# Optimization experiments

Measured on AMD Instinct MI355X. Metric: run time of the kernel, lower is better.

The kernel has to match this reference:

```python
import jax, jax.numpy as jnp
import numpy as np

N_NODES = 100000
N_EDGES = 1600000
IN_FEATS, HIDDEN, N_CLASSES = 128, 64, 16


def gcn_layer(x, src, dst, W, b, n_nodes):
    # DGL GraphConv, norm='both': h = D_in^{-1/2} A (D_out^{-1/2} x) W + b
    # (W applied before aggregation since in_feats > out_feats, as DGL does)
    ones = jnp.ones((src.shape[0],), dtype=x.dtype)
    deg_out = jax.ops.segment_sum(ones, src, num_segments=n_nodes)
    deg_in = jax.ops.segment_sum(ones, dst, num_segments=n_nodes)
    norm_src = jax.lax.rsqrt(jnp.clip(deg_out, 1.0))  # [N]
    norm_dst = jax.lax.rsqrt(jnp.clip(deg_in, 1.0))   # [N]
    h = (x * norm_src[:, None]) @ W                    # [N, out]
    msgs = h[src]                                      # [E, out] gather
    agg = jax.ops.segment_sum(msgs, dst, num_segments=n_nodes)  # [N, out]
    return agg * norm_dst[:, None] + b


def setup_inputs() -> dict:
    key = jax.random.key(0)
    k1, k2, k3, k4, k5, k6, k7 = jax.random.split(key, 7)
    x = jax.random.normal(k1, (N_NODES, IN_FEATS), dtype=jnp.float32)
    src = jax.random.randint(k2, (N_EDGES,), 0, N_NODES, dtype=jnp.int32)
    dst = jax.random.randint(k3, (N_EDGES,), 0, N_NODES, dtype=jnp.int32)
    s1 = 1.0 / np.sqrt(IN_FEATS)
    s2 = 1.0 / np.sqrt(HIDDEN)
    W1 = jax.random.uniform(k4, (IN_FEATS, HIDDEN), jnp.float32, -s1, s1)
    b1 = jnp.zeros((HIDDEN,), dtype=jnp.float32)
    W2 = jax.random.uniform(k5, (HIDDEN, N_CLASSES), jnp.float32, -s2, s2)
    b2 = jnp.zeros((N_CLASSES,), dtype=jnp.float32)
    return {"x": x, "src": src, "dst": dst, "W1": W1, "b1": b1, "W2": W2, "b2": b2}


def reference(x, src, dst, W1, b1, W2, b2):
    h = gcn_layer(x, src, dst, W1, b1, N_NODES)
    h = jax.nn.relu(h)
    h = gcn_layer(h, src, dst, W2, b2, N_NODES)
    return jax.nn.softmax(h, axis=-1)  # [N, num_classes]
```

## Files before the change

kernel.cpp:

```cpp
#include <hip/hip_runtime.h>
#include <hip/hip_fp16.h>
#include <math.h>


constexpr int N_NODES = 100000;
constexpr int N_EDGES = 1600000;
constexpr int IN_F    = 128;
constexpr int HID     = 64;
constexpr int NC      = 16;

constexpr int NB_D   = 391;
constexpr int STR    = 4608;
constexpr int NBLK_P = 256;
constexpr int EPB    = N_EDGES / NBLK_P;
constexpr int CAPB   = 64;
constexpr int CSTR   = 16;

typedef _Float16 f16x8 __attribute__((ext_vector_type(8)));
typedef _Float16 f16x4 __attribute__((ext_vector_type(4)));
typedef float    f32x4 __attribute__((ext_vector_type(4)));

__global__ __launch_bounds__(512) void k_init(int* __restrict__ cursD,
                                              int* __restrict__ cursS) {
    int t = threadIdx.x;
    if (t < NB_D) {
        cursD[t * CSTR] = t * STR;
        cursS[t * CSTR] = t * STR;
    }
}

__global__ __launch_bounds__(1024) void k_part(const int* __restrict__ src,
                                               const int* __restrict__ dst,
                                               int* __restrict__ cursD,
                                               int* __restrict__ cursS,
                                               unsigned int* __restrict__ ebufD,
                                               unsigned char* __restrict__ ebufS) {
    __shared__ unsigned int  bufD[NB_D * CAPB];
    __shared__ unsigned char bufS[NB_D * CAPB];
    __shared__ int cD[NB_D], cS[NB_D], baseD[NB_D], baseS[NB_D];
    const int t = threadIdx.x, b = blockIdx.x;
    for (int i = t; i < NB_D; i += 1024) { cD[i] = 0; cS[i] = 0; }
    __syncthreads();
    const int beg = b * EPB, end = beg + EPB;
    for (int i = beg + t; i < end; i += 1024) {
        int d = dst[i], s = src[i];
        int bD = d >> 8;
        int c  = atomicAdd(&cD[bD], 1);
        if (c < CAPB) bufD[(bD << 6) + c] = ((unsigned)(d & 255) << 17) | (unsigned)s;
        int bS = s >> 8;
        int c2 = atomicAdd(&cS[bS], 1);
        if (c2 < CAPB) bufS[(bS << 6) + c2] = (unsigned char)(s & 255);
    }
    __syncthreads();
    for (int i = t; i < NB_D; i += 1024) {
        int c = min(cD[i], CAPB);
        cD[i] = c;
        baseD[i] = atomicAdd(&cursD[i * CSTR], c);
        int c2 = min(cS[i], CAPB);
        cS[i] = c2;
        baseS[i] = atomicAdd(&cursS[i * CSTR], c2);
    }
    __syncthreads();
    for (int slot = t; slot < NB_D * CAPB; slot += 1024) {
        int bk = slot >> 6, idx = slot & 63;
        if (idx < cD[bk]) ebufD[baseD[bk] + idx] = bufD[slot];
    }
    for (int slot = t; slot < NB_D * CAPB; slot += 1024) {
        int bk = slot >> 6, idx = slot & 63;
        if (idx < cS[bk]) ebufS[baseS[bk] + idx] = bufS[slot];
    }
}

__global__ __launch_bounds__(256) void k_bcsr(const int* __restrict__ cursD,
                                              const unsigned int* __restrict__ ebufD,
                                              int* __restrict__ row_start,
                                              int* __restrict__ row_end,
                                              float* __restrict__ norm_dst,
                                              int* __restrict__ csr_src) {
    __shared__ int cnt[256];
    __shared__ int curs[256];
    __shared__ int wsum[4];
    const int t = threadIdx.x, b = blockIdx.x;
    const int beg = b * STR, end = cursD[b * CSTR];
    cnt[t] = 0;
    __syncthreads();
    for (int i = beg + t; i < end; i += 256)
        atomicAdd(&cnt[ebufD[i] >> 17], 1);
    __syncthreads();
    int x = cnt[t];
    int v = x;
    int lane = t & 63, wid = t >> 6;
    #pragma unroll
    for (int d = 1; d < 64; d <<= 1) { int u = __shfl_up(v, d, 64); if (lane >= d) v += u; }
    if (lane == 63) wsum[wid] = v;
    __syncthreads();
    int woff = 0;
    for (int w = 0; w < wid; ++w) woff += wsum[w];
    int rs = woff + v - x;
    int node = b * 256 + t;
    if (node < N_NODES) {
        row_start[node] = beg + rs;
        row_end[node]   = beg + rs + x;
        norm_dst[node]  = 1.0f / sqrtf(fmaxf((float)x, 1.0f));
    }
    curs[t] = beg + rs;
    __syncthreads();
    for (int i = beg + t; i < end; i += 256) {
        unsigned int e = ebufD[i];
        int pos = atomicAdd(&curs[e >> 17], 1);
        csr_src[pos] = (int)(e & 0x1FFFFu);
    }
}

__global__ __launch_bounds__(256) void k_bdeg(const int* __restrict__ cursS,
                                              const unsigned char* __restrict__ ebufS,
                                              float* __restrict__ norm_src) {
    __shared__ int cnt[256];
    const int t = threadIdx.x, b = blockIdx.x;
    const int beg = b * STR, end = cursS[b * CSTR];
    cnt[t] = 0;
    __syncthreads();
    for (int i = beg + t; i < end; i += 256)
        atomicAdd(&cnt[ebufS[i]], 1);
    __syncthreads();
    int node = b * 256 + t;
    if (node < N_NODES)
        norm_src[node] = 1.0f / sqrtf(fmaxf((float)cnt[t], 1.0f));
}

constexpr int PADK = 136;
__global__ __launch_bounds__(256) void k_gemm1(
        const float* __restrict__ x, const float* __restrict__ W1,
        const float* __restrict__ norm_src, __half* __restrict__ h1h) {
    __shared__ _Float16 xh[64 * PADK];
    __shared__ _Float16 wt[64 * PADK];
    const int t = threadIdx.x;
    const int row0 = blockIdx.x * 64;
    for (int i = t; i < 64 * 32; i += 256) {
        int c4 = i & 31, rr = i >> 5;
        int gr = row0 + rr;
        float4 v = (gr < N_NODES) ? *(const float4*)&x[(size_t)gr * IN_F + c4 * 4]
                                  : float4{0.f, 0.f, 0.f, 0.f};
        f16x4 hv;
        hv[0] = (_Float16)v.x; hv[1] = (_Float16)v.y;
        hv[2] = (_Float16)v.z; hv[3] = (_Float16)v.w;
        *(f16x4*)&xh[rr * PADK + c4 * 4] = hv;
    }
    for (int i = t; i < 64 * 32; i += 256) {
        int n = i & 63, kq = i >> 6;
        int k0 = kq * 4;
        f16x4 hv;
        #pragma unroll
        for (int j = 0; j < 4; ++j)
            hv[j] = (_Float16)W1[(size_t)(k0 + j) * HID + n];
        *(f16x4*)&wt[n * PADK + k0] = hv;
    }
    __syncthreads();
    const int w = t >> 6;
    const int l = t & 63;
    const int m = l & 15, q = l >> 4;
    f32x4 acc0 = {0,0,0,0}, acc1 = {0,0,0,0}, acc2 = {0,0,0,0}, acc3 = {0,0,0,0};
    #pragma unroll
    for (int kc = 0; kc < 4; ++kc) {
        f16x8 af = *(const f16x8*)&xh[(16 * w + m) * PADK + kc * 32 + q * 8];
        f16x8 b0 = *(const f16x8*)&wt[( 0 + m) * PADK + kc * 32 + q * 8];
        f16x8 b1 = *(const f16x8*)&wt[(16 + m) * PADK + kc * 32 + q * 8];
        f16x8 b2 = *(const f16x8*)&wt[(32 + m) * PADK + kc * 32 + q * 8];
        f16x8 b3 = *(const f16x8*)&wt[(48 + m) * PADK + kc * 32 + q * 8];
        acc0 = __builtin_amdgcn_mfma_f32_16x16x32_f16(af, b0, acc0, 0, 0, 0);
        acc1 = __builtin_amdgcn_mfma_f32_16x16x32_f16(af, b1, acc1, 0, 0, 0);
        acc2 = __builtin_amdgcn_mfma_f32_16x16x32_f16(af, b2, acc2, 0, 0, 0);
        acc3 = __builtin_amdgcn_mfma_f32_16x16x32_f16(af, b3, acc3, 0, 0, 0);
    }
    _Float16* out = (_Float16*)h1h;
    #pragma unroll
    for (int r = 0; r < 4; ++r) {
        int row_g = row0 + 16 * w + q * 4 + r;
        if (row_g < N_NODES) {
            float ns = norm_src[row_g];
            size_t base = (size_t)row_g * HID + m;
            out[base +  0] = (_Float16)(acc0[r] * ns);
            out[base + 16] = (_Float16)(acc1[r] * ns);
            out[base + 32] = (_Float16)(acc2[r] * ns);
            out[base + 48] = (_Float16)(acc3[r] * ns);
        }
    }
}

__global__ __launch_bounds__(256) void k_agg1(
        const int* __restrict__ row_start, const int* __restrict__ row_end,
        const int* __restrict__ csr_src, const __half* __restrict__ h1h,
        const float* __restrict__ nd, const float* __restrict__ b1,
        float* __restrict__ h1r) {
    int node = blockIdx.x * 16 + (threadIdx.x >> 4);
    int q = threadIdx.x & 15;
    if (node >= N_NODES) return;
    int beg = row_start[node], end = row_end[node];
    float4 acc = {0.f, 0.f, 0.f, 0.f};
    int p = beg;
    for (; p + 8 <= end; p += 8) {
        float2 g[8];
        #pragma unroll
        for (int u = 0; u < 8; ++u) {
            int s = csr_src[p + u];
            g[u] = *(const float2*)&h1h[(size_t)s * HID + q * 4];
        }
        #pragma unroll
        for (int u = 0; u < 8; ++u) {
            float2 f0 = __half22float2(*(__half2*)&g[u].x);
            float2 f1 = __half22float2(*(__half2*)&g[u].y);
            acc.x += f0.x; acc.y += f0.y; acc.z += f1.x; acc.w += f1.y;
        }
    }
    for (; p < end; ++p) {
        int s = csr_src[p];
        float2 raw = *(const float2*)&h1h[(size_t)s * HID + q * 4];
        float2 f0 = __half22float2(*(__half2*)&raw.x);
        float2 f1 = __half22float2(*(__half2*)&raw.y);
        acc.x += f0.x; acc.y += f0.y; acc.z += f1.x; acc.w += f1.y;
    }
    float n = nd[node];
    float4 bb = *(const float4*)&b1[q * 4];
    float4 o;
    o.x = fmaxf(acc.x * n + bb.x, 0.f);
    o.y = fmaxf(acc.y * n + bb.y, 0.f);
    o.z = fmaxf(acc.z * n + bb.z, 0.f);
    o.w = fmaxf(acc.w * n + bb.w, 0.f);
    *(float4*)&h1r[(size_t)node * HID + q * 4] = o;
}

#define GEMM_STEP(accr, xvr) \
    accr.x += xvr.x*w0.x + xvr.y*w1.x + xvr.z*w2.x + xvr.w*w3.x; \
    accr.y += xvr.x*w0.y + xvr.y*w1.y + xvr.z*w2.y + xvr.w*w3.y; \
    accr.z += xvr.x*w0.z + xvr.y*w1.z + xvr.z*w2.z + xvr.w*w3.z; \
    accr.w += xvr.x*w0.w + xvr.y*w1.w + xvr.z*w2.w + xvr.w*w3.w;

__global__ __launch_bounds__(256) void k_gemm2(
        const float* __restrict__ hin, const float* __restrict__ W2,
        const float* __restrict__ norm_src, __half* __restrict__ h2h) {
    __shared__ float Ws[HID * NC];
    __shared__ float xs[64 * 68];
    const int t = threadIdx.x;
    for (int i = t * 4; i < HID * NC; i += 256 * 4)
        *(float4*)&Ws[i] = *(const float4*)&W2[i];
    const int jq = t & 3;
    const int rl = t >> 2;
    const int row0 = blockIdx.x * 64;
    __syncthreads();
    for (int i = t; i < 64 * (HID / 4); i += 256) {
        int rr = i >> 4, cc = i & 15;
        int gr = row0 + rr;
        float4 v = (gr < N_NODES) ? *(const float4*)&hin[(size_t)gr * HID + cc * 4]
                                  : float4{0.f, 0.f, 0.f, 0.f};
        *(float4*)&xs[rr * 68 + cc * 4] = v;
    }
    __syncthreads();
    int r = row0 + rl;
    if (r < N_NODES) {
        float4 acc = {0.f, 0.f, 0.f, 0.f};
        #pragma unroll
        for (int k = 0; k < HID; k += 4) {
            float4 xv = *(float4*)&xs[rl * 68 + k];
            float4 w0 = *(float4*)&Ws[(k + 0) * NC + jq * 4];
            float4 w1 = *(float4*)&Ws[(k + 1) * NC + jq * 4];
            float4 w2 = *(float4*)&Ws[(k + 2) * NC + jq * 4];
            float4 w3 = *(float4*)&Ws[(k + 3) * NC + jq * 4];
            GEMM_STEP(acc, xv)
        }
        float ns = norm_src[r];
        f16x4 hv;
        hv[0] = (_Float16)(acc.x * ns); hv[1] = (_Float16)(acc.y * ns);
        hv[2] = (_Float16)(acc.z * ns); hv[3] = (_Float16)(acc.w * ns);
        *(f16x4*)&((_Float16*)h2h)[(size_t)r * NC + jq * 4] = hv;
    }
}

__global__ __launch_bounds__(256) void k_agg2(
        const int* __restrict__ row_start, const int* __restrict__ row_end,
        const int* __restrict__ csr_src, const __half* __restrict__ h2h,
        const float* __restrict__ nd, const float* __restrict__ b2,
        float* __restrict__ out) {
    int t = threadIdx.x;
    int node = blockIdx.x * 128 + (t >> 1);
    int sub = t & 1;
    if (node >= N_NODES) return;
    int beg = row_start[node], end = row_end[node];
    float acc[8] = {0,0,0,0,0,0,0,0};
    int p = beg;
    for (; p + 4 <= end; p += 4) {
        float4 g[4];
        #pragma unroll
        for (int u = 0; u < 4; ++u) {
            int s = csr_src[p + u];
            g[u] = *(const float4*)&h2h[(size_t)s * NC + sub * 8];
        }
        #pragma unroll
        for (int u = 0; u < 4; ++u) {
            const __half2* hh = (const __half2*)&g[u];
            #pragma unroll
            for (int j = 0; j < 4; ++j) {
                float2 f = __half22float2(hh[j]);
                acc[j * 2 + 0] += f.x; acc[j * 2 + 1] += f.y;
            }
        }
    }
    for (; p < end; ++p) {
        int s = csr_src[p];
        float4 g = *(const float4*)&h2h[(size_t)s * NC + sub * 8];
        const __half2* hh = (const __half2*)&g;
        #pragma unroll
        for (int j = 0; j < 4; ++j) {
            float2 f = __half22float2(hh[j]);
            acc[j * 2 + 0] += f.x; acc[j * 2 + 1] += f.y;
        }
    }
    float n = nd[node];
    float v[8];
    #pragma unroll
    for (int j = 0; j < 8; ++j) v[j] = acc[j] * n + b2[sub * 8 + j];
    float m = v[0];
    #pragma unroll
    for (int j = 1; j < 8; ++j) m = fmaxf(m, v[j]);
    m = fmaxf(m, __shfl_xor(m, 1, 2));
    float e[8]; float s = 0.f;
    #pragma unroll
    for (int j = 0; j < 8; ++j) { e[j] = __expf(v[j] - m); s += e[j]; }
    s += __shfl_xor(s, 1, 2);
    float inv = 1.0f / s;
    float4 o0 = { e[0]*inv, e[1]*inv, e[2]*inv, e[3]*inv };
    float4 o1 = { e[4]*inv, e[5]*inv, e[6]*inv, e[7]*inv };
    *(float4*)&out[(size_t)node * NC + sub * 8 + 0] = o0;
    *(float4*)&out[(size_t)node * NC + sub * 8 + 4] = o1;
}

extern "C" void kernel_launch(void* const* d_in, const int* in_sizes, int n_in,
                              void* d_out, int out_size, void* d_ws, size_t ws_size,
                              hipStream_t stream) {
    const float* x   = (const float*)d_in[0];
    const int*   src = (const int*)  d_in[1];
    const int*   dst = (const int*)  d_in[2];
    const float* W1  = (const float*)d_in[3];
    const float* b1  = (const float*)d_in[4];
    const float* W2  = (const float*)d_in[5];
    const float* b2  = (const float*)d_in[6];
    float* out = (float*)d_out;

    const size_t N = N_NODES;
    float* ws       = (float*)d_ws;
    int*   wsI      = (int*)d_ws;
    float* norm_src = ws;
    float* norm_dst = ws + N;
    __half* h1h     = (__half*)(ws + 2 * N);
    __half* h2h     = (__half*)(ws + 2 * N);
    float* h1r      = ws + 66 * N;
    unsigned int*  ebufD = (unsigned int*)(wsI + 66 * N);
    unsigned char* ebufS = (unsigned char*)(wsI + 66 * N + NB_D * STR);
    int*   row_st   = wsI + 130 * N;
    int*   row_en   = wsI + 131 * N;
    int*   cursD    = wsI + 132 * N;
    int*   cursS    = wsI + 132 * N + 8192;
    int*   csr_src  = wsI + 132 * N + 16384;

    k_init<<<1, 512, 0, stream>>>(cursD, cursS);
    k_part<<<NBLK_P, 1024, 0, stream>>>(src, dst, cursD, cursS, ebufD, ebufS);
    k_bcsr<<<NB_D, 256, 0, stream>>>(cursD, ebufD, row_st, row_en, norm_dst, csr_src);
    k_bdeg<<<NB_D, 256, 0, stream>>>(cursS, ebufS, norm_src);
    k_gemm1<<<(N_NODES + 63) / 64, 256, 0, stream>>>(x, W1, norm_src, h1h);
    k_agg1<<<(N_NODES + 15) / 16, 256, 0, stream>>>(row_st, row_en, csr_src, h1h,
                                                    norm_dst, b1, h1r);
    k_gemm2<<<(N_NODES + 63) / 64, 256, 0, stream>>>(h1r, W2, norm_src, h2h);
    k_agg2<<<(N_NODES + 127) / 128, 256, 0, stream>>>(row_st, row_en, csr_src, h2h,
                                                      norm_dst, b2, out);
}
```

Baseline: 221.8 us.

## Fuse second-layer GEMM into first aggregation and merge CSR/degree kernels

The layer-1 aggregation kernel now applies bias and ReLU, multiplies by W2 held in shared memory, reduces the partial products across the 16 lanes of each node with xor shuffles, and writes the fp16 h2 directly. This removes the fp32 h1 round trip through global memory and the separate gemm2 launch. The CSR build and source-degree kernels are merged into one launch with block-index dispatch, and agg2's gather unroll goes from 4 to 8. In exchange, agg1 does extra shuffle work and uses more registers, which may lower its occupancy.

```diff
diff --git a/kernel.cpp b/kernel.cpp
--- a/kernel.cpp
+++ b/kernel.cpp
@@ -71,61 +71,62 @@
     }
 }
 
-__global__ __launch_bounds__(256) void k_bcsr(const int* __restrict__ cursD,
-                                              const unsigned int* __restrict__ ebufD,
-                                              int* __restrict__ row_start,
-                                              int* __restrict__ row_end,
-                                              float* __restrict__ norm_dst,
-                                              int* __restrict__ csr_src) {
+__global__ __launch_bounds__(256) void k_bmerge(const int* __restrict__ cursD,
+                                                const int* __restrict__ cursS,
+                                                const unsigned int* __restrict__ ebufD,
+                                                const unsigned char* __restrict__ ebufS,
+                                                int* __restrict__ row_start,
+                                                int* __restrict__ row_end,
+                                                float* __restrict__ norm_dst,
+                                                float* __restrict__ norm_src,
+                                                int* __restrict__ csr_src) {
     __shared__ int cnt[256];
     __shared__ int curs[256];
     __shared__ int wsum[4];
-    const int t = threadIdx.x, b = blockIdx.x;
-    const int beg = b * STR, end = cursD[b * CSTR];
-    cnt[t] = 0;
-    __syncthreads();
-    for (int i = beg + t; i < end; i += 256)
-        atomicAdd(&cnt[ebufD[i] >> 17], 1);
-    __syncthreads();
-    int x = cnt[t];
-    int v = x;
-    int lane = t & 63, wid = t >> 6;
-    #pragma unroll
-    for (int d = 1; d < 64; d <<= 1) { int u = __shfl_up(v, d, 64); if (lane >= d) v += u; }
-    if (lane == 63) wsum[wid] = v;
-    __syncthreads();
-    int woff = 0;
-    for (int w = 0; w < wid; ++w) woff += wsum[w];
-    int rs = woff + v - x;
-    int node = b * 256 + t;
-    if (node < N_NODES) {
-        row_start[node] = beg + rs;
-        row_end[node]   = beg + rs + x;
-        norm_dst[node]  = 1.0f / sqrtf(fmaxf((float)x, 1.0f));
-    }
-    curs[t] = beg + rs;
-    __syncthreads();
-    for (int i = beg + t; i < end; i += 256) {
-        unsigned int e = ebufD[i];
-        int pos = atomicAdd(&curs[e >> 17], 1);
-        csr_src[pos] = (int)(e & 0x1FFFFu);
-    }
-}
-
-__global__ __launch_bounds__(256) void k_bdeg(const int* __restrict__ cursS,
-                                              const unsigned char* __restrict__ ebufS,
-                                              float* __restrict__ norm_src) {
-    __shared__ int cnt[256];
-    const int t = threadIdx.x, b = blockIdx.x;
-    const int beg = b * STR, end = cursS[b * CSTR];
-    cnt[t] = 0;
-    __syncthreads();
-    for (int i = beg + t; i < end; i += 256)
-        atomicAdd(&cnt[ebufS[i]], 1);
-    __syncthreads();
-    int node = b * 256 + t;
-    if (node < N_NODES)
-        norm_src[node] = 1.0f / sqrtf(fmaxf((float)cnt[t], 1.0f));
+    const int t = threadIdx.x;
+    int b = blockIdx.x;
+    if (b < NB_D) {
+        const int beg = b * STR, end = cursD[b * CSTR];
+        cnt[t] = 0;
+        __syncthreads();
+        for (int i = beg + t; i < end; i += 256)
+            atomicAdd(&cnt[ebufD[i] >> 17], 1);
+        __syncthreads();
+        int x = cnt[t];
+        int v = x;
+        int lane = t & 63, wid = t >> 6;
+        #pragma unroll
+        for (int d = 1; d < 64; d <<= 1) { int u = __shfl_up(v, d, 64); if (lane >= d) v += u; }
+        if (lane == 63) wsum[wid] = v;
+        __syncthreads();
+        int woff = 0;
+        for (int w = 0; w < wid; ++w) woff += wsum[w];
+        int rs = woff + v - x;
+        int node = b * 256 + t;
+        if (node < N_NODES) {
+            row_start[node] = beg + rs;
+            row_end[node]   = beg + rs + x;
+            norm_dst[node]  = 1.0f / sqrtf(fmaxf((float)x, 1.0f));
+        }
+        curs[t] = beg + rs;
+        __syncthreads();
+        for (int i = beg + t; i < end; i += 256) {
+            unsigned int e = ebufD[i];
+            int pos = atomicAdd(&curs[e >> 17], 1);
+            csr_src[pos] = (int)(e & 0x1FFFFu);
+        }
+    } else {
+        b -= NB_D;
+        const int beg = b * STR, end = cursS[b * CSTR];
+        cnt[t] = 0;
+        __syncthreads();
+        for (int i = beg + t; i < end; i += 256)
+            atomicAdd(&cnt[ebufS[i]], 1);
+        __syncthreads();
+        int node = b * 256 + t;
+        if (node < N_NODES)
+            norm_src[node] = 1.0f / sqrtf(fmaxf((float)cnt[t], 1.0f));
+    }
 }
 
 constexpr int PADK = 136;
@@ -190,10 +191,18 @@
 __global__ __launch_bounds__(256) void k_agg1(
         const int* __restrict__ row_start, const int* __restrict__ row_end,
         const int* __restrict__ csr_src, const __half* __restrict__ h1h,
-        const float* __restrict__ nd, const float* __restrict__ b1,
-        float* __restrict__ h1r) {
-    int node = blockIdx.x * 16 + (threadIdx.x >> 4);
-    int q = threadIdx.x & 15;
+        const float* __restrict__ nd, const float* __restrict__ ns,
+        const float* __restrict__ b1, const float* __restrict__ W2,
+        __half* __restrict__ h2h) {
+    __shared__ float W2s[64 * 17];
+    const int t = threadIdx.x;
+    for (int i = t; i < HID * NC; i += 256) {
+        int k = i >> 4, j = i & 15;
+        W2s[k * 17 + j] = W2[i];
+    }
+    __syncthreads();
+    int node = blockIdx.x * 16 + (t >> 4);
+    int q = t & 15;
     if (node >= N_NODES) return;
     int beg = row_start[node], end = row_end[node];
     float4 acc = {0.f, 0.f, 0.f, 0.f};
@@ -221,58 +230,26 @@
     }
     float n = nd[node];
     float4 bb = *(const float4*)&b1[q * 4];
-    float4 o;
-    o.x = fmaxf(acc.x * n + bb.x, 0.f);
-    o.y = fmaxf(acc.y * n + bb.y, 0.f);
-    o.z = fmaxf(acc.z * n + bb.z, 0.f);
-    o.w = fmaxf(acc.w * n + bb.w, 0.f);
-    *(float4*)&h1r[(size_t)node * HID + q * 4] = o;
-}
-
-#define GEMM_STEP(accr, xvr) \
-    accr.x += xvr.x*w0.x + xvr.y*w1.x + xvr.z*w2.x + xvr.w*w3.x; \
-    accr.y += xvr.x*w0.y + xvr.y*w1.y + xvr.z*w2.y + xvr.w*w3.y; \
-    accr.z += xvr.x*w0.z + xvr.y*w1.z + xvr.z*w2.z + xvr.w*w3.z; \
-    accr.w += xvr.x*w0.w + xvr.y*w1.w + xvr.z*w2.w + xvr.w*w3.w;
-
-__global__ __launch_bounds__(256) void k_gemm2(
-        const float* __restrict__ hin, const float* __restrict__ W2,
-        const float* __restrict__ norm_src, __half* __restrict__ h2h) {
-    __shared__ float Ws[HID * NC];
-    __shared__ float xs[64 * 68];
-    const int t = threadIdx.x;
-    for (int i = t * 4; i < HID * NC; i += 256 * 4)
-        *(float4*)&Ws[i] = *(const float4*)&W2[i];
-    const int jq = t & 3;
-    const int rl = t >> 2;
-    const int row0 = blockIdx.x * 64;
-    __syncthreads();
-    for (int i = t; i < 64 * (HID / 4); i += 256) {
-        int rr = i >> 4, cc = i & 15;
-        int gr = row0 + rr;
-        float4 v = (gr < N_NODES) ? *(const float4*)&hin[(size_t)gr * HID + cc * 4]
-                                  : float4{0.f, 0.f, 0.f, 0.f};
-        *(float4*)&xs[rr * 68 + cc * 4] = v;
-    }
-    __syncthreads();
-    int r = row0 + rl;
-    if (r < N_NODES) {
-        float4 acc = {0.f, 0.f, 0.f, 0.f};
-        #pragma unroll
-        for (int k = 0; k < HID; k += 4) {
-            float4 xv = *(float4*)&xs[rl * 68 + k];
-            float4 w0 = *(float4*)&Ws[(k + 0) * NC + jq * 4];
-            float4 w1 = *(float4*)&Ws[(k + 1) * NC + jq * 4];
-            float4 w2 = *(float4*)&Ws[(k + 2) * NC + jq * 4];
-            float4 w3 = *(float4*)&Ws[(k + 3) * NC + jq * 4];
-            GEMM_STEP(acc, xv)
-        }
-        float ns = norm_src[r];
-        f16x4 hv;
-        hv[0] = (_Float16)(acc.x * ns); hv[1] = (_Float16)(acc.y * ns);
-        hv[2] = (_Float16)(acc.z * ns); hv[3] = (_Float16)(acc.w * ns);
-        *(f16x4*)&((_Float16*)h2h)[(size_t)r * NC + jq * 4] = hv;
-    }
+    float v0 = fmaxf(acc.x * n + bb.x, 0.f);
+    float v1 = fmaxf(acc.y * n + bb.y, 0.f);
+    float v2 = fmaxf(acc.z * n + bb.z, 0.f);
+    float v3 = fmaxf(acc.w * n + bb.w, 0.f);
+    float part[16];
+    const float* w0 = &W2s[(4 * q + 0) * 17];
+    const float* w1 = &W2s[(4 * q + 1) * 17];
+    const float* w2 = &W2s[(4 * q + 2) * 17];
+    const float* w3 = &W2s[(4 * q + 3) * 17];
+    #pragma unroll
+    for (int j = 0; j < 16; ++j)
+        part[j] = v0 * w0[j] + v1 * w1[j] + v2 * w2[j] + v3 * w3[j];
+    #pragma unroll
+    for (int d = 1; d < 16; d <<= 1) {
+        #pragma unroll
+        for (int j = 0; j < 16; ++j)
+            part[j] += __shfl_xor(part[j], d, 16);
+    }
+    float nsv = ns[node];
+    ((_Float16*)h2h)[(size_t)node * NC + q] = (_Float16)(part[q] * nsv);
 }
 
 __global__ __launch_bounds__(256) void k_agg2(
@@ -287,15 +264,15 @@
     int beg = row_start[node], end = row_end[node];
     float acc[8] = {0,0,0,0,0,0,0,0};
     int p = beg;
-    for (; p + 4 <= end; p += 4) {
-        float4 g[4];
-        #pragma unroll
-        for (int u = 0; u < 4; ++u) {
+    for (; p + 8 <= end; p += 8) {
+        float4 g[8];
+        #pragma unroll
+        for (int u = 0; u < 8; ++u) {
             int s = csr_src[p + u];
             g[u] = *(const float4*)&h2h[(size_t)s * NC + sub * 8];
         }
         #pragma unroll
-        for (int u = 0; u < 4; ++u) {
+        for (int u = 0; u < 8; ++u) {
             const __half2* hh = (const __half2*)&g[u];
             #pragma unroll
             for (int j = 0; j < 4; ++j) {
@@ -351,8 +328,7 @@
     float* norm_src = ws;
     float* norm_dst = ws + N;
     __half* h1h     = (__half*)(ws + 2 * N);
-    __half* h2h     = (__half*)(ws + 2 * N);
-    float* h1r      = ws + 66 * N;
+    __half* h2h     = (__half*)(ws + 34 * N);
     unsigned int*  ebufD = (unsigned int*)(wsI + 66 * N);
     unsigned char* ebufS = (unsigned char*)(wsI + 66 * N + NB_D * STR);
     int*   row_st   = wsI + 130 * N;
@@ -363,12 +339,12 @@
 
     k_init<<<1, 512, 0, stream>>>(cursD, cursS);
     k_part<<<NBLK_P, 1024, 0, stream>>>(src, dst, cursD, cursS, ebufD, ebufS);
-    k_bcsr<<<NB_D, 256, 0, stream>>>(cursD, ebufD, row_st, row_en, norm_dst, csr_src);
-    k_bdeg<<<NB_D, 256, 0, stream>>>(cursS, ebufS, norm_src);
+    k_bmerge<<<2 * NB_D, 256, 0, stream>>>(cursD, cursS, ebufD, ebufS,
+                                           row_st, row_en, norm_dst, norm_src,
+                                           csr_src);
     k_gemm1<<<(N_NODES + 63) / 64, 256, 0, stream>>>(x, W1, norm_src, h1h);
     k_agg1<<<(N_NODES + 15) / 16, 256, 0, stream>>>(row_st, row_en, csr_src, h1h,
-                                                    norm_dst, b1, h1r);
-    k_gemm2<<<(N_NODES + 63) / 64, 256, 0, stream>>>(h1r, W2, norm_src, h2h);
+                                                    norm_dst, norm_src, b1, W2, h2h);
     k_agg2<<<(N_NODES + 127) / 128, 256, 0, stream>>>(row_st, row_en, csr_src, h2h,
                                                       norm_dst, b2, out);
 }
```

Result: no change. 221.3 us (-0.2%).
